# Optimization experiments

Hardware: AMD Instinct MI355X
Metric: run time of the kernel (lower is better)

The kernel has to match this reference:

```python
import jax, jax.numpy as jnp
import numpy as np

K = 76          # model dim = 6 + 30 + 30 + 10 (concat of modality embeddings)
H = 8           # heads; per-head dim == K (wide attention variant)
D = 6           # depth
T = 1024        # seq_length (frames)
B = 8           # batch
C = 2           # num_classes
EPS = 1e-5


def setup_inputs() -> dict:
    key = jax.random.key(0)
    ks = jax.random.split(key, 24)
    rn = lambda k, shape, s=0.02: (jax.random.normal(k, shape, jnp.float32) * s)
    return {
        # forward inputs (per-frame multimodal features)
        "v": jax.random.normal(ks[0], (B, T, 6), jnp.float32),
        "x": jax.random.normal(ks[1], (B, T, 137), jnp.float32),
        "y": jax.random.normal(ks[2], (B, T, 113), jnp.float32),
        "z": jax.random.normal(ks[3], (B, T, 35), jnp.float32),
        # modality embed linears (stored (in, out); torch does x @ W.T)
        "W_hp": rn(ks[4], (6, 6)),     "b_hp": jnp.zeros((6,), jnp.float32),
        "W_lm": rn(ks[5], (137, 30)),  "b_lm": jnp.zeros((30,), jnp.float32),
        "W_el": rn(ks[6], (113, 30)),  "b_el": jnp.zeros((30,), jnp.float32),
        "W_au": rn(ks[7], (35, 10)),   "b_au": jnp.zeros((10,), jnp.float32),
        "pos_emb": rn(ks[8], (T, K)),
        # per-block params stacked over depth for lax.scan
        "Wq": rn(ks[9], (D, K, H * K)),
        "Wk": rn(ks[10], (D, K, H * K)),
        "Wv": rn(ks[11], (D, K, H * K)),
        "Wu": rn(ks[12], (D, H * K, K)), "bu": jnp.zeros((D, K), jnp.float32),
        "ln1_s": jnp.ones((D, K), jnp.float32), "ln1_b": jnp.zeros((D, K), jnp.float32),
        "W1": rn(ks[13], (D, K, 4 * K)), "b1": jnp.zeros((D, 4 * K), jnp.float32),
        "W2": rn(ks[14], (D, 4 * K, K)), "b2": jnp.zeros((D, K), jnp.float32),
        "ln2_s": jnp.ones((D, K), jnp.float32), "ln2_b": jnp.zeros((D, K), jnp.float32),
        "W_out": rn(ks[15], (K, C)), "b_out": jnp.zeros((C,), jnp.float32),
    }


def _layernorm(h, s, b):
    mu = jnp.mean(h, axis=-1, keepdims=True)
    var = jnp.mean(jnp.square(h - mu), axis=-1, keepdims=True)
    return (h - mu) * jax.lax.rsqrt(var + EPS) * s + b


def reference(v, x, y, z,
              W_hp, b_hp, W_lm, b_lm, W_el, b_el, W_au, b_au,
              pos_emb, Wq, Wk, Wv, Wu, bu, ln1_s, ln1_b,
              W1, b1, W2, b2, ln2_s, ln2_b, W_out, b_out):
    b, t = v.shape[0], v.shape[1]
    tokens = jnp.concatenate([
        v @ W_hp + b_hp,
        x @ W_lm + b_lm,
        y @ W_el + b_el,
        z @ W_au + b_au,
    ], axis=2)                                   # (b, t, K)
    h = tokens + pos_emb[None, :, :]
    scale = 1.0 / np.sqrt(K)                     # dot / sqrt(e), e == k

    def block(hh, p):
        wq, wk, wv, wu, bu_, l1s, l1b, w1, b1_, w2, b2_, l2s, l2b = p
        # (b, t, H*K) -> (b, H, t, K); per-head dim is full K here
        q = (hh @ wq).reshape(b, t, H, K).transpose(0, 2, 1, 3)
        k_ = (hh @ wk).reshape(b, t, H, K).transpose(0, 2, 1, 3)
        vv = (hh @ wv).reshape(b, t, H, K).transpose(0, 2, 1, 3)
        dot = jax.nn.softmax(jnp.einsum('bhte,bhse->bhts', q, k_) * scale, axis=-1)
        att = jnp.einsum('bhts,bhse->bhte', dot, vv)        # (b, H, t, K)
        att = att.transpose(0, 2, 1, 3).reshape(b, t, H * K)
        att = att @ wu + bu_                                # unify heads -> (b, t, K)
        h1 = _layernorm(att + hh, l1s, l1b)
        ff = jax.nn.relu(h1 @ w1 + b1_) @ w2 + b2_
        return _layernorm(ff + h1, l2s, l2b), None

    h, _ = jax.lax.scan(
        block, h,
        (Wq, Wk, Wv, Wu, bu, ln1_s, ln1_b, W1, b1, W2, b2, ln2_s, ln2_b))
    return h @ W_out + b_out                     # (b, t, num_classes)
```

## Files before the change

kernel.cpp:

```cpp
#include <hip/hip_runtime.h>
#include <hip/hip_bf16.h>
#include <math.h>

#define B_   8
#define T_   1024
#define K_   76
#define KP_  96
#define H_   8
#define D_   6
#define C_   2
#define HK_  608
#define QKLD_ 640
#define FF_  304
#define FFP_ 320
#define EK_  320
#define BT_  8192
#define EPS_ 1e-5f
#define SCL2_ (0.11470786693528088f * 1.4426950408889634f)

typedef unsigned short u16;
typedef unsigned int u32;
typedef short bf16x8 __attribute__((ext_vector_type(8)));
typedef float f32x4 __attribute__((ext_vector_type(4)));

__device__ __forceinline__ u16 f2b(float f) {
  __hip_bfloat16 h = __float2bfloat16(f);
  return *reinterpret_cast<u16*>(&h);
}
__device__ __forceinline__ float b2f(u16 u) {
  __hip_bfloat16 h = *reinterpret_cast<__hip_bfloat16*>(&u);
  return __bfloat162float(h);
}
__device__ __forceinline__ u32 pack2(float a, float b) {
  __hip_bfloat162 t = __float22bfloat162_rn(make_float2(a, b));
  return *reinterpret_cast<u32*>(&t);
}

#define PER_L_ 304128ULL
__global__ __launch_bounds__(256) void wconv_kernel(
    const float* __restrict__ Wq, const float* __restrict__ Wk, const float* __restrict__ Wv,
    const float* __restrict__ Wu, const float* __restrict__ W1, const float* __restrict__ W2,
    u16* __restrict__ WT) {
  __shared__ float Ls[32][65];
  int zz = blockIdx.y;
  int d = zz / 6, wt = zz % 6;
  const float* in; int Kd, Nsrc, Nalloc, Kp; u16* out;
  size_t lb = (size_t)d * PER_L_;
  switch (wt) {
    case 0: in = Wq + (size_t)d*K_*HK_; Kd=K_;  Nsrc=HK_; Nalloc=640; Kp=KP_;  out = WT + lb;          break;
    case 1: in = Wk + (size_t)d*K_*HK_; Kd=K_;  Nsrc=HK_; Nalloc=640; Kp=KP_;  out = WT + lb + 61440;  break;
    case 2: in = Wv + (size_t)d*K_*HK_; Kd=K_;  Nsrc=HK_; Nalloc=640; Kp=KP_;  out = WT + lb + 122880; break;
    case 3: in = Wu + (size_t)d*HK_*K_; Kd=HK_; Nsrc=K_;  Nalloc=96;  Kp=HK_;  out = WT + lb + 184320; break;
    case 4: in = W1 + (size_t)d*K_*FF_; Kd=K_;  Nsrc=FF_; Nalloc=320; Kp=KP_;  out = WT + lb + 242688; break;
    default:in = W2 + (size_t)d*FF_*K_; Kd=FF_; Nsrc=K_;  Nalloc=96;  Kp=FFP_; out = WT + lb + 273408; break;
  }
  int tiles_k = Kp / 32;
  int tiles_n = (Nalloc + 63) / 64;
  int tile = blockIdx.x;
  if (tile >= tiles_k * tiles_n) return;
  int tn = tile / tiles_k, tk = tile % tiles_k;
  int n0 = tn * 64, k0 = tk * 32;
  for (int i = threadIdx.x; i < 2048; i += 256) {
    int kk = i >> 6, nn = i & 63;
    int gk = k0 + kk, gn = n0 + nn;
    int srccol = gn;
    if (wt < 3) {
      int hh8 = gn / 80, ft = gn - hh8 * 80;
      srccol = (ft < 76) ? (hh8 * 76 + ft) : -1;
    }
    Ls[kk][nn] = (gk < Kd && srccol >= 0 && srccol < Nsrc) ? in[(size_t)gk * Nsrc + srccol] : 0.f;
  }
  __syncthreads();
  for (int i = threadIdx.x; i < 2048; i += 256) {
    int nn = i >> 5, kk = i & 31;
    int gn = n0 + nn;
    if (gn < Nalloc) out[(size_t)gn * Kp + k0 + kk] = f2b(Ls[kk][nn]);
  }
}

__global__ void wembed_kernel(const float* __restrict__ W_hp, const float* __restrict__ b_hp,
                              const float* __restrict__ W_lm, const float* __restrict__ b_lm,
                              const float* __restrict__ W_el, const float* __restrict__ b_el,
                              const float* __restrict__ W_au, const float* __restrict__ b_au,
                              u16* __restrict__ WE) {
  int idx = blockIdx.x * 256 + threadIdx.x;
  if (idx >= 96 * EK_) return;
  int n = idx / EK_, kk = idx % EK_;
  float val = 0.f;
  if (n < 76) {
    if (kk < 6) { if (n < 6) val = W_hp[kk * 6 + n]; }
    else if (kk < 143) { int i = kk - 6; if (n >= 6 && n < 36) val = W_lm[i * 30 + (n - 6)]; }
    else if (kk < 256) { int i = kk - 143; if (n >= 36 && n < 66) val = W_el[i * 30 + (n - 36)]; }
    else if (kk < 291) { int i = kk - 256; if (n >= 66) val = W_au[i * 10 + (n - 66)]; }
    else if (kk == 291) {
      val = (n < 6) ? b_hp[n] : (n < 36) ? b_lm[n - 6] : (n < 66) ? b_el[n - 36] : b_au[n - 66];
    }
  }
  WE[idx] = f2b(val);
}

__global__ void pack_kernel(const float* __restrict__ v, const float* __restrict__ x,
                            const float* __restrict__ y, const float* __restrict__ z,
                            u16* __restrict__ xin) {
  int idx = blockIdx.x * 256 + threadIdx.x;
  if (idx >= BT_ * (EK_ / 2)) return;
  int bt = idx / (EK_ / 2), dc = idx % (EK_ / 2);
  int c0 = dc * 2;
  auto fetch = [&](int c) -> float {
    if (c < 6) return v[bt * 6 + c];
    if (c < 143) return x[bt * 137 + c - 6];
    if (c < 256) return y[bt * 113 + c - 143];
    if (c < 291) return z[bt * 35 + c - 256];
    if (c == 291) return 1.0f;
    return 0.f;
  };
  ((u32*)xin)[idx] = pack2(fetch(c0), fetch(c0 + 1));
}

template<int RT, int CT, int KSTEPS, int RELU, int LNFUSE, int TPB>
__global__ __launch_bounds__(TPB) void gemm_kernel(
    const u16* __restrict__ A, int lda,
    const u16* __restrict__ Wt, int ldw, unsigned long long wstride,
    const float* __restrict__ bias,
    u16* __restrict__ Cc, int ldc, int N,
    int ksplit, int klen, unsigned long long osplit,
    float cs,
    u16* __restrict__ vbt,
    const float* __restrict__ pos,
    const u16* __restrict__ res,
    const float* __restrict__ lns,
    const float* __restrict__ lnb) {
  __shared__ u16 Bs[CT * 16 * 56];
  const int tid = threadIdx.x;
  const int w = tid >> 6, lane = tid & 63;
  const int r = lane & 15, g = lane >> 4;
  const int n0 = blockIdx.x * CT * 16;
  const int m0 = blockIdx.y * (TPB / 64) * 16 * RT;
  const int z = blockIdx.z;
  const int k0 = z * ksplit;
  const int kend = k0 + klen;
  const u16* Wz = Wt + (size_t)z * wstride;
  const float* bias_eff = (z == 0) ? bias : nullptr;
  const float csz = (z == 0) ? cs : 1.f;
  u16* Cz = Cc + (size_t)z * osplit;
  constexpr int NB = (CT * 64 + TPB - 1) / TPB;

  const f32x4 fz = {0.f, 0.f, 0.f, 0.f};
  f32x4 acc[RT][CT];
  #pragma unroll
  for (int rt = 0; rt < RT; rt++)
    #pragma unroll
    for (int ct = 0; ct < CT; ct++) acc[rt][ct] = fz;

  bf16x8 a_all[RT][KSTEPS];
  #pragma unroll
  for (int rt = 0; rt < RT; rt++) {
    const u16* arow = A + (size_t)(m0 + (w * RT + rt) * 16 + r) * lda;
    #pragma unroll
    for (int ks = 0; ks < KSTEPS; ks++) {
      int kA = k0 + ks * 32 + g * 8;
      if (kA < kend) a_all[rt][ks] = *(const bf16x8*)(arow + kA);
      else a_all[rt][ks] = bf16x8{0, 0, 0, 0, 0, 0, 0, 0};
    }
  }

  uint4 bpre[NB];
  auto loadB = [&](int ks) {
    int kk = k0 + ks * 32;
    #pragma unroll
    for (int i0 = 0; i0 < NB; i0++) {
      int idx = tid + i0 * TPB;
      bpre[i0] = make_uint4(0, 0, 0, 0);
      if (idx < CT * 64) {
        int nn = idx >> 2, kc = idx & 3;
        if (kk + kc * 8 < kend)
          bpre[i0] = *(const uint4*)(Wz + (size_t)(n0 + nn) * ldw + kk + kc * 8);
      }
    }
  };
  loadB(0);

  for (int ks = 0; ks < KSTEPS; ks++) {
    __syncthreads();
    #pragma unroll
    for (int i0 = 0; i0 < NB; i0++) {
      int idx = tid + i0 * TPB;
      if (idx < CT * 64) {
        int nn = idx >> 2, kc = idx & 3;
        *(uint4*)&Bs[nn * 56 + (((kc ^ (nn & 3)) << 3))] = bpre[i0];
      }
    }
    __syncthreads();
    if (ks + 1 < KSTEPS) loadB(ks + 1);
    #pragma unroll
    for (int ct = 0; ct < CT; ct++) {
      bf16x8 bb = *(const bf16x8*)&Bs[(ct * 16 + r) * 56 + (((g ^ (r & 3)) << 3))];
      #pragma unroll
      for (int rt = 0; rt < RT; rt++)
        acc[rt][ct] = __builtin_amdgcn_mfma_f32_16x16x32_bf16(a_all[rt][ks], bb, acc[rt][ct], 0, 0, 0);
    }
  }

  if (LNFUSE) {
    #pragma unroll
    for (int reg = 0; reg < 4; reg++) {
      int row = m0 + w * 16 + g * 4 + reg;
      const u16* resr = res + (size_t)row * KP_;
      float vals[CT];
      float s = 0.f, s2 = 0.f;
      #pragma unroll
      for (int ct = 0; ct < CT; ct++) {
        int col = ct * 16 + r;
        float val = 0.f;
        if (col < N) {
          val = acc[0][ct][reg] + bias[col] + b2f(resr[col]);
          s += val; s2 += val * val;
        }
        vals[ct] = val;
      }
      #pragma unroll
      for (int m = 1; m < 16; m <<= 1) { s += __shfl_xor(s, m); s2 += __shfl_xor(s2, m); }
      float mu = s * (1.f / 76.f);
      float rstd = rsqrtf(s2 * (1.f / 76.f) - mu * mu + EPS_);
      u16* outr = Cz + (size_t)row * ldc;
      #pragma unroll
      for (int ct = 0; ct < CT; ct++) {
        int col = ct * 16 + r;
        u16 ov = 0;
        if (col < N) ov = f2b((vals[ct] - mu) * rstd * lns[col] + lnb[col]);
        if (col < ldc) outr[col] = ov;
      }
    }
  } else if (vbt && z == 2) {
    #pragma unroll
    for (int rt = 0; rt < RT; rt++) {
      #pragma unroll
      for (int ct = 0; ct < CT; ct++) {
        int feat = ct * 16 + r;
        int token = m0 + (w * RT + rt) * 16 + g * 4;
        int bb_ = token >> 10, tt = token & 1023;
        ushort4 pk;
        if (feat < 76) {
          pk.x = f2b(acc[rt][ct][0]); pk.y = f2b(acc[rt][ct][1]);
          pk.z = f2b(acc[rt][ct][2]); pk.w = f2b(acc[rt][ct][3]);
        } else {
          pk = make_ushort4(0, 0, 0, 0);
        }
        *(ushort4*)(vbt + (((size_t)(bb_ * 8 + blockIdx.x) * 80 + feat) << 10) + tt) = pk;
      }
    }
  } else {
    #pragma unroll
    for (int rt = 0; rt < RT; rt++) {
      #pragma unroll
      for (int ct = 0; ct < CT; ct++) {
        int col = n0 + ct * 16 + r;
        if (col < ldc) {
          #pragma unroll
          for (int reg = 0; reg < 4; reg++) {
            int row = m0 + (w * RT + rt) * 16 + g * 4 + reg;
            float val = acc[rt][ct][reg] * csz;
            if (bias_eff && col < N) val += bias_eff[col];
            if (pos && col < N) val += pos[(row & (T_ - 1)) * K_ + col];
            if (RELU) val = fmaxf(val, 0.f);
            Cz[(size_t)row * ldc + col] = f2b(val);
          }
        }
      }
    }
  }
}

__global__ __launch_bounds__(256, 3) void attn_kernel(const u16* __restrict__ q,
                                                      const u16* __restrict__ k,
                                                      const u16* __restrict__ vbt,
                                                      u16* __restrict__ att) {
  __shared__ u16 Ks[64 * 104];
  __shared__ u16 Vs[80 * 72];
  __shared__ u32 Psw[128 * 36];
  const int bid = blockIdx.x;
  const int hh = bid & 7, b = (bid >> 3) & 7, qt = bid >> 6;
  const int tid = threadIdx.x;
  const int w = tid >> 6, lane = tid & 63;
  const int r = lane & 15, g = lane >> 4;
  const int qbase = b * T_ + qt * 128;

  bf16x8 aq[2][3];
  #pragma unroll
  for (int rt = 0; rt < 2; rt++) {
    const u16* qsrc = q + (size_t)(qbase + w * 32 + rt * 16 + r) * QKLD_ + hh * 80;
    #pragma unroll
    for (int ks = 0; ks < 3; ks++) {
      int e0 = ks * 32 + g * 8;
      aq[rt][ks] = (e0 < 80) ? *(const bf16x8*)(qsrc + e0) : bf16x8{0, 0, 0, 0, 0, 0, 0, 0};
    }
  }

  const int krow = tid >> 2, kq4 = tid & 3;
  uint4 kpre[3], vpre[3];
  auto stage_load = [&](int kt) {
    const int kb = b * T_ + kt * 64;
    const u16* ksrc = k + (size_t)(kb + krow) * QKLD_ + hh * 80;
    #pragma unroll
    for (int i = 0; i < 3; i++) {
      int c = kq4 + 4 * i;
      kpre[i] = (c < 10) ? *(const uint4*)(ksrc + c * 8) : make_uint4(0, 0, 0, 0);
    }
    const u16* vsrc = vbt + (((size_t)(b * 8 + hh) * 80) << 10) + kt * 64;
    #pragma unroll
    for (int p = 0; p < 3; p++) {
      int idx = tid + p * 256;
      vpre[p] = (idx < 640) ? *(const uint4*)(vsrc + ((size_t)(idx >> 3) << 10) + (idx & 7) * 8)
                            : make_uint4(0, 0, 0, 0);
    }
  };
  auto stage_write = [&]() {
    #pragma unroll
    for (int i = 0; i < 3; i++) {
      int c = kq4 + 4 * i;
      *(uint4*)&Ks[krow * 104 + c * 8] = kpre[i];
    }
    #pragma unroll
    for (int p = 0; p < 3; p++) {
      int idx = tid + p * 256;
      if (idx < 640)
        *(uint4*)&Vs[(idx >> 3) * 72 + (idx & 7) * 8] = vpre[p];
    }
  };

  u32* Pw = Psw + w * 32 * 36;

  const f32x4 fz = {0.f, 0.f, 0.f, 0.f};
  f32x4 o[2][5];
  float ls[2] = {0.f, 0.f};
  #pragma unroll
  for (int rt = 0; rt < 2; rt++)
    #pragma unroll
    for (int i = 0; i < 5; i++) o[rt][i] = fz;

  stage_load(0);

  for (int kt = 0; kt < 16; kt++) {
    __syncthreads();
    stage_write();
    __syncthreads();
    if (kt < 15) stage_load(kt + 1);

    f32x4 st[2][4];
    #pragma unroll
    for (int ct = 0; ct < 4; ct++) { st[0][ct] = fz; st[1][ct] = fz; }
    __builtin_amdgcn_s_setprio(1);
    #pragma unroll
    for (int ct = 0; ct < 4; ct++) {
      #pragma unroll
      for (int ks = 0; ks < 3; ks++) {
        bf16x8 ak = *(const bf16x8*)&Ks[(ct * 16 + r) * 104 + ks * 32 + g * 8];
        st[0][ct] = __builtin_amdgcn_mfma_f32_16x16x32_bf16(ak, aq[0][ks], st[0][ct], 0, 0, 0);
        st[1][ct] = __builtin_amdgcn_mfma_f32_16x16x32_bf16(ak, aq[1][ks], st[1][ct], 0, 0, 0);
      }
    }
    __builtin_amdgcn_s_setprio(0);

    #pragma unroll
    for (int rt = 0; rt < 2; rt++) {
      float rs = 0.f;
      u32 pk[8];
      #pragma unroll
      for (int ct = 0; ct < 4; ct++) {
        float p0 = exp2f(st[rt][ct][0]), p1 = exp2f(st[rt][ct][1]);
        float p2 = exp2f(st[rt][ct][2]), p3 = exp2f(st[rt][ct][3]);
        rs += (p0 + p1) + (p2 + p3);
        pk[ct * 2] = pack2(p0, p1);
        pk[ct * 2 + 1] = pack2(p2, p3);
      }
      ls[rt] += rs;
      u32* pw = Pw + (rt * 16 + r) * 36;
      #pragma unroll
      for (int ct = 0; ct < 4; ct++)
        *(uint2*)(pw + ct * 8 + g * 2) = make_uint2(pk[ct * 2], pk[ct * 2 + 1]);
    }

    bf16x8 pa[2][2];
    #pragma unroll
    for (int rt = 0; rt < 2; rt++) {
      const u32* pr = Pw + (rt * 16 + r) * 36;
      #pragma unroll
      for (int ks = 0; ks < 2; ks++) {
        uint4 t = *(const uint4*)(pr + ks * 16 + g * 4);
        pa[rt][ks] = *reinterpret_cast<bf16x8*>(&t);
      }
    }
    __builtin_amdgcn_s_setprio(1);
    #pragma unroll
    for (int ks = 0; ks < 2; ks++) {
      #pragma unroll
      for (int c5 = 0; c5 < 5; c5++) {
        bf16x8 av = *(const bf16x8*)&Vs[(c5 * 16 + r) * 72 + ks * 32 + g * 8];
        #pragma unroll
        for (int rt = 0; rt < 2; rt++)
          o[rt][c5] = __builtin_amdgcn_mfma_f32_16x16x32_bf16(av, pa[rt][ks], o[rt][c5], 0, 0, 0);
      }
    }
    __builtin_amdgcn_s_setprio(0);
  }

  #pragma unroll
  for (int rt = 0; rt < 2; rt++) {
    ls[rt] += __shfl_xor(ls[rt], 16);
    ls[rt] += __shfl_xor(ls[rt], 32);
    float inv = 1.f / ls[rt];
    int token = qbase + w * 32 + rt * 16 + r;
    #pragma unroll
    for (int c5 = 0; c5 < 5; c5++) {
      if (c5 == 4 && g == 3) continue;
      ushort4 pk4;
      pk4.x = f2b(o[rt][c5][0] * inv);
      pk4.y = f2b(o[rt][c5][1] * inv);
      pk4.z = f2b(o[rt][c5][2] * inv);
      pk4.w = f2b(o[rt][c5][3] * inv);
      *(ushort4*)&att[(size_t)token * HK_ + hh * 76 + c5 * 16 + g * 4] = pk4;
    }
  }
}

__global__ void out_kernel(const u16* __restrict__ h, const float* __restrict__ W,
                           const float* __restrict__ bias, float* __restrict__ out) {
  int bt = blockIdx.x * 256 + threadIdx.x;
  if (bt >= BT_) return;
  const u32* hr = (const u32*)(h + (size_t)bt * KP_);
  float acc0 = bias[0], acc1 = bias[1];
  #pragma unroll 4
  for (int d = 0; d < 38; d++) {
    u32 h2 = hr[d];
    float f0 = b2f((u16)(h2 & 0xffff)), f1 = b2f((u16)(h2 >> 16));
    acc0 += f0 * W[(2 * d) * 2] + f1 * W[(2 * d + 1) * 2];
    acc1 += f0 * W[(2 * d) * 2 + 1] + f1 * W[(2 * d + 1) * 2 + 1];
  }
  out[bt * 2] = acc0;
  out[bt * 2 + 1] = acc1;
}

extern "C" void kernel_launch(void* const* d_in, const int* in_sizes, int n_in,
                              void* d_out, int out_size, void* d_ws, size_t ws_size,
                              hipStream_t stream) {
  const float* v    = (const float*)d_in[0];
  const float* x    = (const float*)d_in[1];
  const float* y    = (const float*)d_in[2];
  const float* z    = (const float*)d_in[3];
  const float* W_hp = (const float*)d_in[4];
  const float* b_hp = (const float*)d_in[5];
  const float* W_lm = (const float*)d_in[6];
  const float* b_lm = (const float*)d_in[7];
  const float* W_el = (const float*)d_in[8];
  const float* b_el = (const float*)d_in[9];
  const float* W_au = (const float*)d_in[10];
  const float* b_au = (const float*)d_in[11];
  const float* pos  = (const float*)d_in[12];
  const float* Wq   = (const float*)d_in[13];
  const float* Wk   = (const float*)d_in[14];
  const float* Wv   = (const float*)d_in[15];
  const float* Wu   = (const float*)d_in[16];
  const float* bu   = (const float*)d_in[17];
  const float* ln1s = (const float*)d_in[18];
  const float* ln1b = (const float*)d_in[19];
  const float* W1   = (const float*)d_in[20];
  const float* b1   = (const float*)d_in[21];
  const float* W2   = (const float*)d_in[22];
  const float* b2   = (const float*)d_in[23];
  const float* ln2s = (const float*)d_in[24];
  const float* ln2b = (const float*)d_in[25];
  const float* Wout = (const float*)d_in[26];
  const float* bout = (const float*)d_in[27];

  u16* ws  = (u16*)d_ws;
  u16* WT  = ws;
  u16* WE  = WT + 1824768;
  u16* h   = WE + 30720;
  u16* xin = h + 786432;
  u16* qb  = xin + 2621440;
  u16* kb  = qb + 5242880;
  u16* vbt = kb + 5242880;
  u16* att = vbt + 5242880;
  u16* h1  = kb;
  u16* ff  = att;

  wconv_kernel<<<dim3(38, 36), 256, 0, stream>>>(Wq, Wk, Wv, Wu, W1, W2, WT);
  wembed_kernel<<<(96 * EK_ + 255) / 256, 256, 0, stream>>>(
      W_hp, b_hp, W_lm, b_lm, W_el, b_el, W_au, b_au, WE);
  pack_kernel<<<(BT_ * (EK_ / 2) + 255) / 256, 256, 0, stream>>>(v, x, y, z, xin);
  gemm_kernel<1, 6, 10, 0, 0, 128><<<dim3(1, 256, 1), 128, 0, stream>>>(
      xin, EK_, WE, EK_, 0ULL, nullptr, h, KP_, K_, 0, EK_, 0ULL,
      1.f, nullptr, pos, nullptr, nullptr, nullptr);

  for (int d = 0; d < D_; d++) {
    u16* WTd = WT + (size_t)d * PER_L_;
    const float* bu_d = bu + (size_t)d * K_;
    const float* l1s  = ln1s + (size_t)d * K_;
    const float* l1b  = ln1b + (size_t)d * K_;
    const float* b1_d = b1 + (size_t)d * FF_;
    const float* b2_d = b2 + (size_t)d * K_;
    const float* l2s  = ln2s + (size_t)d * K_;
    const float* l2b  = ln2b + (size_t)d * K_;

    gemm_kernel<2, 5, 3, 0, 0, 256><<<dim3(8, 64, 3), 256, 0, stream>>>(
        h, KP_, WTd, KP_, 61440ULL, nullptr, qb, QKLD_, QKLD_, 0, KP_, 5242880ULL,
        SCL2_, vbt, nullptr, nullptr, nullptr, nullptr);
    attn_kernel<<<dim3(512), 256, 0, stream>>>(qb, kb, vbt, att);
    gemm_kernel<1, 6, 19, 0, 1, 128><<<dim3(1, 256, 1), 128, 0, stream>>>(
        att, HK_, WTd + 184320, HK_, 0ULL, bu_d, h1, KP_, K_, 0, HK_, 0ULL,
        1.f, nullptr, nullptr, h, l1s, l1b);
    gemm_kernel<2, 5, 3, 1, 0, 256><<<dim3(4, 64, 1), 256, 0, stream>>>(
        h1, KP_, WTd + 242688, KP_, 0ULL, b1_d, ff, FFP_, FF_, 0, KP_, 0ULL,
        1.f, nullptr, nullptr, nullptr, nullptr, nullptr);
    gemm_kernel<1, 6, 10, 0, 1, 128><<<dim3(1, 256, 1), 128, 0, stream>>>(
        ff, FFP_, WTd + 273408, FFP_, 0ULL, b2_d, h, KP_, K_, 0, FFP_, 0ULL,
        1.f, nullptr, nullptr, h1, l2s, l2b);
  }

  out_kernel<<<(BT_ + 255) / 256, 256, 0, stream>>>(h, Wout, bout, (float*)d_out);
}
```

Measured before the change: 641.4 us.

## Fuse head-unify, LayerNorm, FFN and second LayerNorm into one kernel

Replaces three per-layer GEMM launches (unify-heads with LN1, FFN up-projection with ReLU, FFN down-projection with LN2) with a single ffn_kernel. Each 64-thread block handles 16 tokens and keeps h1 and the ReLU activations in shared memory, so the h1 and ff intermediates no longer make a round trip through global memory and two launches per layer go away. The trade-off is small single-wave blocks with heavy register use (20 accumulators plus 20 B fragments loaded straight from global), which may limit latency hiding. The block reads residual h and then overwrites h in place; this appears safe because each block touches only its own rows.

```diff
diff --git a/kernel.cpp b/kernel.cpp
--- a/kernel.cpp
+++ b/kernel.cpp
@@ -117,7 +117,7 @@
   ((u32*)xin)[idx] = pack2(fetch(c0), fetch(c0 + 1));
 }
 
-template<int RT, int CT, int KSTEPS, int RELU, int LNFUSE, int TPB>
+template<int RT, int CT, int KSTEPS, int RELU, int TPB>
 __global__ __launch_bounds__(TPB) void gemm_kernel(
     const u16* __restrict__ A, int lda,
     const u16* __restrict__ Wt, int ldw, unsigned long long wstride,
@@ -126,10 +126,7 @@
     int ksplit, int klen, unsigned long long osplit,
     float cs,
     u16* __restrict__ vbt,
-    const float* __restrict__ pos,
-    const u16* __restrict__ res,
-    const float* __restrict__ lns,
-    const float* __restrict__ lnb) {
+    const float* __restrict__ pos) {
   __shared__ u16 Bs[CT * 16 * 56];
   const int tid = threadIdx.x;
   const int w = tid >> 6, lane = tid & 63;
@@ -201,37 +198,7 @@
     }
   }
 
-  if (LNFUSE) {
-    #pragma unroll
-    for (int reg = 0; reg < 4; reg++) {
-      int row = m0 + w * 16 + g * 4 + reg;
-      const u16* resr = res + (size_t)row * KP_;
-      float vals[CT];
-      float s = 0.f, s2 = 0.f;
-      #pragma unroll
-      for (int ct = 0; ct < CT; ct++) {
-        int col = ct * 16 + r;
-        float val = 0.f;
-        if (col < N) {
-          val = acc[0][ct][reg] + bias[col] + b2f(resr[col]);
-          s += val; s2 += val * val;
-        }
-        vals[ct] = val;
-      }
-      #pragma unroll
-      for (int m = 1; m < 16; m <<= 1) { s += __shfl_xor(s, m); s2 += __shfl_xor(s2, m); }
-      float mu = s * (1.f / 76.f);
-      float rstd = rsqrtf(s2 * (1.f / 76.f) - mu * mu + EPS_);
-      u16* outr = Cz + (size_t)row * ldc;
-      #pragma unroll
-      for (int ct = 0; ct < CT; ct++) {
-        int col = ct * 16 + r;
-        u16 ov = 0;
-        if (col < N) ov = f2b((vals[ct] - mu) * rstd * lns[col] + lnb[col]);
-        if (col < ldc) outr[col] = ov;
-      }
-    }
-  } else if (vbt && z == 2) {
+  if (vbt && z == 2) {
     #pragma unroll
     for (int rt = 0; rt < RT; rt++) {
       #pragma unroll
@@ -267,6 +234,178 @@
           }
         }
       }
+    }
+  }
+}
+
+__global__ __launch_bounds__(64) void ffn_kernel(
+    const u16* __restrict__ att, const u16* __restrict__ WuT, const float* __restrict__ bu,
+    const u16* __restrict__ hres, const float* __restrict__ l1s, const float* __restrict__ l1b,
+    const u16* __restrict__ W1T, const float* __restrict__ b1,
+    const u16* __restrict__ W2T, const float* __restrict__ b2,
+    const float* __restrict__ l2s, const float* __restrict__ l2b,
+    u16* __restrict__ hout) {
+  __shared__ u16 Bs[6 * 16 * 56];
+  __shared__ u16 h1s[16 * 104];
+  __shared__ u16 ffs[16 * 328];
+  const int lane = threadIdx.x & 63;
+  const int r = lane & 15, g = lane >> 4;
+  const int m0 = blockIdx.x * 16;
+  const f32x4 fz = {0.f, 0.f, 0.f, 0.f};
+
+  u16 resv[4][6];
+  #pragma unroll
+  for (int reg = 0; reg < 4; reg++)
+    #pragma unroll
+    for (int ct = 0; ct < 6; ct++)
+      resv[reg][ct] = hres[(size_t)(m0 + g * 4 + reg) * KP_ + ct * 16 + r];
+
+  bf16x8 a1[19];
+  {
+    const u16* arow = att + (size_t)(m0 + r) * HK_;
+    #pragma unroll
+    for (int ks = 0; ks < 19; ks++) a1[ks] = *(const bf16x8*)(arow + ks * 32 + g * 8);
+  }
+  f32x4 acc1[6];
+  #pragma unroll
+  for (int ct = 0; ct < 6; ct++) acc1[ct] = fz;
+  {
+    uint4 bpre[6];
+    auto loadB1 = [&](int ks) {
+      #pragma unroll
+      for (int i0 = 0; i0 < 6; i0++) {
+        int idx = lane + i0 * 64;
+        int nn = idx >> 2, kc = idx & 3;
+        bpre[i0] = *(const uint4*)(WuT + (size_t)nn * HK_ + ks * 32 + kc * 8);
+      }
+    };
+    loadB1(0);
+    for (int ks = 0; ks < 19; ks++) {
+      #pragma unroll
+      for (int i0 = 0; i0 < 6; i0++) {
+        int idx = lane + i0 * 64;
+        int nn = idx >> 2, kc = idx & 3;
+        *(uint4*)&Bs[nn * 56 + ((kc ^ (nn & 3)) << 3)] = bpre[i0];
+      }
+      if (ks + 1 < 19) loadB1(ks + 1);
+      #pragma unroll
+      for (int ct = 0; ct < 6; ct++) {
+        bf16x8 bb = *(const bf16x8*)&Bs[(ct * 16 + r) * 56 + ((g ^ (r & 3)) << 3)];
+        acc1[ct] = __builtin_amdgcn_mfma_f32_16x16x32_bf16(a1[ks], bb, acc1[ct], 0, 0, 0);
+      }
+    }
+  }
+  #pragma unroll
+  for (int reg = 0; reg < 4; reg++) {
+    float vals[6];
+    float s = 0.f, s2 = 0.f;
+    #pragma unroll
+    for (int ct = 0; ct < 6; ct++) {
+      int col = ct * 16 + r;
+      float val = 0.f;
+      if (col < K_) {
+        val = acc1[ct][reg] + bu[col] + b2f(resv[reg][ct]);
+        s += val; s2 += val * val;
+      }
+      vals[ct] = val;
+    }
+    #pragma unroll
+    for (int m = 1; m < 16; m <<= 1) { s += __shfl_xor(s, m); s2 += __shfl_xor(s2, m); }
+    float mu = s * (1.f / 76.f);
+    float rstd = rsqrtf(s2 * (1.f / 76.f) - mu * mu + EPS_);
+    #pragma unroll
+    for (int ct = 0; ct < 6; ct++) {
+      int col = ct * 16 + r;
+      u16 ov = 0;
+      if (col < K_) ov = f2b((vals[ct] - mu) * rstd * l1s[col] + l1b[col]);
+      h1s[(g * 4 + reg) * 104 + col] = ov;
+    }
+  }
+
+  bf16x8 a2[3];
+  #pragma unroll
+  for (int ks = 0; ks < 3; ks++)
+    a2[ks] = *(const bf16x8*)&h1s[r * 104 + ks * 32 + g * 8];
+  f32x4 acc2[20];
+  #pragma unroll
+  for (int ct = 0; ct < 20; ct++) acc2[ct] = fz;
+  #pragma unroll
+  for (int ks = 0; ks < 3; ks++) {
+    bf16x8 bb[20];
+    #pragma unroll
+    for (int ct = 0; ct < 20; ct++)
+      bb[ct] = *(const bf16x8*)(W1T + (size_t)(ct * 16 + r) * KP_ + ks * 32 + g * 8);
+    #pragma unroll
+    for (int ct = 0; ct < 20; ct++)
+      acc2[ct] = __builtin_amdgcn_mfma_f32_16x16x32_bf16(a2[ks], bb[ct], acc2[ct], 0, 0, 0);
+  }
+  #pragma unroll
+  for (int reg = 0; reg < 4; reg++)
+    #pragma unroll
+    for (int ct = 0; ct < 20; ct++) {
+      int col = ct * 16 + r;
+      float val = acc2[ct][reg] + ((col < FF_) ? b1[col] : 0.f);
+      ffs[(g * 4 + reg) * 328 + col] = f2b(fmaxf(val, 0.f));
+    }
+
+  bf16x8 a3[10];
+  #pragma unroll
+  for (int ks = 0; ks < 10; ks++)
+    a3[ks] = *(const bf16x8*)&ffs[r * 328 + ks * 32 + g * 8];
+  f32x4 acc3[6];
+  #pragma unroll
+  for (int ct = 0; ct < 6; ct++) acc3[ct] = fz;
+  {
+    uint4 bpre[6];
+    auto loadB3 = [&](int ks) {
+      #pragma unroll
+      for (int i0 = 0; i0 < 6; i0++) {
+        int idx = lane + i0 * 64;
+        int nn = idx >> 2, kc = idx & 3;
+        bpre[i0] = *(const uint4*)(W2T + (size_t)nn * FFP_ + ks * 32 + kc * 8);
+      }
+    };
+    loadB3(0);
+    for (int ks = 0; ks < 10; ks++) {
+      #pragma unroll
+      for (int i0 = 0; i0 < 6; i0++) {
+        int idx = lane + i0 * 64;
+        int nn = idx >> 2, kc = idx & 3;
+        *(uint4*)&Bs[nn * 56 + ((kc ^ (nn & 3)) << 3)] = bpre[i0];
+      }
+      if (ks + 1 < 10) loadB3(ks + 1);
+      #pragma unroll
+      for (int ct = 0; ct < 6; ct++) {
+        bf16x8 bb = *(const bf16x8*)&Bs[(ct * 16 + r) * 56 + ((g ^ (r & 3)) << 3)];
+        acc3[ct] = __builtin_amdgcn_mfma_f32_16x16x32_bf16(a3[ks], bb, acc3[ct], 0, 0, 0);
+      }
+    }
+  }
+  #pragma unroll
+  for (int reg = 0; reg < 4; reg++) {
+    float vals[6];
+    float s = 0.f, s2 = 0.f;
+    #pragma unroll
+    for (int ct = 0; ct < 6; ct++) {
+      int col = ct * 16 + r;
+      float val = 0.f;
+      if (col < K_) {
+        val = acc3[ct][reg] + b2[col] + b2f(h1s[(g * 4 + reg) * 104 + col]);
+        s += val; s2 += val * val;
+      }
+      vals[ct] = val;
+    }
+    #pragma unroll
+    for (int m = 1; m < 16; m <<= 1) { s += __shfl_xor(s, m); s2 += __shfl_xor(s2, m); }
+    float mu = s * (1.f / 76.f);
+    float rstd = rsqrtf(s2 * (1.f / 76.f) - mu * mu + EPS_);
+    u16* outr = hout + (size_t)(m0 + g * 4 + reg) * KP_;
+    #pragma unroll
+    for (int ct = 0; ct < 6; ct++) {
+      int col = ct * 16 + r;
+      u16 ov = 0;
+      if (col < K_) ov = f2b((vals[ct] - mu) * rstd * l2s[col] + l2b[col]);
+      outr[col] = ov;
     }
   }
 }
@@ -481,16 +620,15 @@
   u16* kb  = qb + 5242880;
   u16* vbt = kb + 5242880;
   u16* att = vbt + 5242880;
-  u16* h1  = kb;
-  u16* ff  = att;
+  u16* h1  = att + 4980736;
 
   wconv_kernel<<<dim3(38, 36), 256, 0, stream>>>(Wq, Wk, Wv, Wu, W1, W2, WT);
   wembed_kernel<<<(96 * EK_ + 255) / 256, 256, 0, stream>>>(
       W_hp, b_hp, W_lm, b_lm, W_el, b_el, W_au, b_au, WE);
   pack_kernel<<<(BT_ * (EK_ / 2) + 255) / 256, 256, 0, stream>>>(v, x, y, z, xin);
-  gemm_kernel<1, 6, 10, 0, 0, 128><<<dim3(1, 256, 1), 128, 0, stream>>>(
+  gemm_kernel<1, 6, 10, 0, 128><<<dim3(1, 256, 1), 128, 0, stream>>>(
       xin, EK_, WE, EK_, 0ULL, nullptr, h, KP_, K_, 0, EK_, 0ULL,
-      1.f, nullptr, pos, nullptr, nullptr, nullptr);
+      1.f, nullptr, pos);
 
   for (int d = 0; d < D_; d++) {
     u16* WTd = WT + (size_t)d * PER_L_;
@@ -502,19 +640,13 @@
     const float* l2s  = ln2s + (size_t)d * K_;
     const float* l2b  = ln2b + (size_t)d * K_;
 
-    gemm_kernel<2, 5, 3, 0, 0, 256><<<dim3(8, 64, 3), 256, 0, stream>>>(
+    gemm_kernel<2, 5, 3, 0, 256><<<dim3(8, 64, 3), 256, 0, stream>>>(
         h, KP_, WTd, KP_, 61440ULL, nullptr, qb, QKLD_, QKLD_, 0, KP_, 5242880ULL,
-        SCL2_, vbt, nullptr, nullptr, nullptr, nullptr);
+        SCL2_, vbt, nullptr);
     attn_kernel<<<dim3(512), 256, 0, stream>>>(qb, kb, vbt, att);
-    gemm_kernel<1, 6, 19, 0, 1, 128><<<dim3(1, 256, 1), 128, 0, stream>>>(
-        att, HK_, WTd + 184320, HK_, 0ULL, bu_d, h1, KP_, K_, 0, HK_, 0ULL,
-        1.f, nullptr, nullptr, h, l1s, l1b);
-    gemm_kernel<2, 5, 3, 1, 0, 256><<<dim3(4, 64, 1), 256, 0, stream>>>(
-        h1, KP_, WTd + 242688, KP_, 0ULL, b1_d, ff, FFP_, FF_, 0, KP_, 0ULL,
-        1.f, nullptr, nullptr, nullptr, nullptr, nullptr);
-    gemm_kernel<1, 6, 10, 0, 1, 128><<<dim3(1, 256, 1), 128, 0, stream>>>(
-        ff, FFP_, WTd + 273408, FFP_, 0ULL, b2_d, h, KP_, K_, 0, FFP_, 0ULL,
-        1.f, nullptr, nullptr, h1, l2s, l2b);
+    ffn_kernel<<<dim3(512), 64, 0, stream>>>(
+        att, WTd + 184320, bu_d, h, l1s, l1b,
+        WTd + 242688, b1_d, WTd + 273408, b2_d, l2s, l2b, h);
   }
 
   out_kernel<<<(BT_ + 255) / 256, 256, 0, stream>>>(h, Wout, bout, (float*)d_out);
```

After: 571.3 us. 1.12x faster.
